# Kernel optimization log

Measured on AMD Instinct MI355X. Metric: run time of the kernel, lower is better.

## Reference

```python
import jax, jax.numpy as jnp
import numpy as np

BIG = 1e9
EPS_BETA = 1e-6
EPS_BN = 1e-5

N_NODES = 50000
N_EDGES = 800000
IN_DIM = 128
OUT_DIM = 128


def setup_inputs() -> dict:
    key = jax.random.key(0)
    ks = jax.random.split(key, 8)
    h = jax.random.normal(ks[0], (N_NODES, IN_DIM), dtype=jnp.float32)
    src = jax.random.randint(ks[1], (N_EDGES,), 0, N_NODES, dtype=jnp.int32)
    dst = jax.random.randint(ks[2], (N_EDGES,), 0, N_NODES, dtype=jnp.int32)
    sigma_GD = jax.random.uniform(ks[3], (N_EDGES,), dtype=jnp.float32)
    fc_w = jax.random.normal(ks[4], (IN_DIM, OUT_DIM), dtype=jnp.float32) / np.sqrt(IN_DIM)
    fc_b = jax.random.normal(ks[5], (OUT_DIM,), dtype=jnp.float32) * 0.01
    attn_w = jax.random.normal(ks[6], (2 * OUT_DIM, 1), dtype=jnp.float32) / np.sqrt(2 * OUT_DIM)
    attn_b = jax.random.normal(ks[7], (1,), dtype=jnp.float32) * 0.01
    bn_gamma = jnp.ones((OUT_DIM,), dtype=jnp.float32)
    bn_beta = jnp.zeros((OUT_DIM,), dtype=jnp.float32)
    return {"h": h, "src": src, "dst": dst, "sigma_GD": sigma_GD,
            "fc_w": fc_w, "fc_b": fc_b, "attn_w": attn_w, "attn_b": attn_b,
            "bn_gamma": bn_gamma, "bn_beta": bn_beta}


def reference(h, src, dst, sigma_GD, fc_w, fc_b, attn_w, attn_b, bn_gamma, bn_beta):
    n = h.shape[0]
    # node projection
    z = h @ fc_w + fc_b                                   # [N, D]
    z = jnp.where(jnp.isinf(z), BIG, z)
    # per-edge attention logits: concat(src,dst) @ W == src@W1 + dst@W2 (avoid concat materialization)
    d = z.shape[1]
    w_src, w_dst = attn_w[:d], attn_w[d:]
    z_src = z[src]                                        # [E, D]
    a = z_src @ w_src + z[dst] @ w_dst + attn_b           # [E, 1]
    a = jnp.where(jnp.isinf(a), BIG, a)
    e = jax.nn.leaky_relu(a, negative_slope=0.01)[:, 0]   # [E]
    # segment softmax over incoming edges (mailbox softmax)
    m = jax.ops.segment_max(e, dst, num_segments=n)       # [N]
    ex = jnp.exp(e - m[dst])
    denom = jax.ops.segment_sum(ex, dst, num_segments=n)  # [N]
    alpha = ex / denom[dst]                               # [E]
    # beta: sigma_GD normalized per destination node
    bsum = jax.ops.segment_sum(sigma_GD, dst, num_segments=n)
    beta = sigma_GD / (bsum[dst] + EPS_BETA)              # [E]
    # weighted scatter-sum of source features
    h_new = jax.ops.segment_sum((alpha * beta)[:, None] * z_src, dst, num_segments=n)  # [N, D]
    h_new = jnp.where(jnp.isinf(h_new), BIG, h_new)
    # BatchNorm1d (training-mode batch stats, biased variance, as torch does)
    mu = h_new.mean(axis=0)
    var = ((h_new - mu) ** 2).mean(axis=0)
    h_bn = (h_new - mu) * jax.lax.rsqrt(var + EPS_BN) * bn_gamma + bn_beta
    return jax.nn.elu(h_bn)
```

## Files before the change

kernel.cpp:

```cpp
#include <hip/hip_runtime.h>
#include <hip/hip_fp16.h>
#include <math.h>

#define N_NODES 50000
#define N_EDGES 800000
#define BIGV 1000000000.0f
#define NBLK_GEMM 3125
#define CHUNK 1024
#define NCHUNK 782
#define NCH4 784
#define NBUCKET 1563
#define NBK4 1564
#define BMAX 768
#define OVFSTRIDE 1024

typedef _Float16 half8 __attribute__((ext_vector_type(8)));
typedef float floatx4 __attribute__((ext_vector_type(4)));

__device__ __forceinline__ float clampinf(float x) { return isinf(x) ? BIGV : x; }

__device__ __forceinline__ void barrier_lgkm_only() {
    __builtin_amdgcn_sched_barrier(0);
    asm volatile("s_waitcnt lgkmcnt(0)" ::: "memory");
    __builtin_amdgcn_s_barrier();
    __builtin_amdgcn_sched_barrier(0);
}

__global__ __launch_bounds__(256) void k_prep(const float* __restrict__ W,
                                              __half* __restrict__ wt,
                                              float* __restrict__ bns,
                                              const int* __restrict__ dst,
                                              int* __restrict__ countsT)
{
    __shared__ int hist[NBK4];
    const int t = threadIdx.x;
    const int idx = blockIdx.x * 256 + t;
    if (idx < 16384) {
        int n = idx >> 7, k = idx & 127;
        wt[idx] = __float2half(W[k * 128 + n]);
    }
    if (idx < 256) bns[idx] = 0.f;
    for (int i = t; i < NBK4; i += 256) hist[i] = 0;
    __syncthreads();
    const int base = blockIdx.x * CHUNK;
    for (int i = t; i < CHUNK; i += 256) {
        int e = base + i;
        if (e < N_EDGES) atomicAdd(&hist[dst[e] >> 5], 1);
    }
    __syncthreads();
    for (int i = t; i < NBK4; i += 256)
        countsT[(size_t)i * NCH4 + blockIdx.x] = hist[i];
}

__global__ __launch_bounds__(256) void k_off(const int* __restrict__ countsT,
                                             int* __restrict__ cursC,
                                             int* __restrict__ btot)
{
    const int wv = (blockIdx.x << 2) + (threadIdx.x >> 6);
    const int l = threadIdx.x & 63;
    if (wv >= NBUCKET) {
        if (l == 0 && wv < NBK4) btot[wv] = 0;
        return;
    }
    const int* row = countsT + (size_t)wv * NCH4;
    int carry = 0;
    #pragma unroll
    for (int p = 0; p < 13; ++p) {
        const int c = p * 64 + l;
        const int v = (c < NCHUNK) ? row[c] : 0;
        int x = v;
        #pragma unroll
        for (int o = 1; o < 64; o <<= 1) {
            int u = __shfl_up(x, o);
            if (l >= o) x += u;
        }
        if (c < NCHUNK) cursC[(size_t)c * NBK4 + wv] = carry + x - v;
        carry += __shfl(x, 63);
    }
    if (l == 0) btot[wv] = carry;
}

__global__ __launch_bounds__(256) void k_gemm(
    const float* __restrict__ h, const __half* __restrict__ wt,
    const float* __restrict__ bias, const float* __restrict__ attn_w,
    __half* __restrict__ zh, float* __restrict__ sv, float* __restrict__ tv)
{
    __shared__ _Float16 hA[16][136];
    __shared__ float spart[4][16], tpart[4][16];

    const int tid = threadIdx.x;
    const int lane = tid & 63;
    const int wv = tid >> 6;
    const int l16 = lane & 15;
    const int oct = lane >> 4;
    const int n0 = wv << 5;
    const int node0 = blockIdx.x << 4;

    {
        const float4* h4 = (const float4*)(h + (size_t)node0 * 128);
        for (int i = tid; i < 512; i += 256) {
            int r = i >> 5, c4 = i & 31;
            float4 v = h4[i];
            union { __half2 h2[2]; uint2 u; } pk;
            pk.h2[0] = __floats2half2_rn(v.x, v.y);
            pk.h2[1] = __floats2half2_rn(v.z, v.w);
            *(uint2*)&hA[r][c4 << 2] = pk.u;
        }
    }

    half8 bfrag[4][2];
    #pragma unroll
    for (int kk = 0; kk < 4; ++kk)
        #pragma unroll
        for (int t = 0; t < 2; ++t)
            bfrag[kk][t] = *(const half8*)(wt + (size_t)(n0 + t * 16 + l16) * 128
                                              + kk * 32 + oct * 8);

    const float bv0 = bias[n0 + l16],         bv1 = bias[n0 + 16 + l16];
    const float ws0 = attn_w[n0 + l16],       ws1 = attn_w[n0 + 16 + l16];
    const float wd0 = attn_w[128 + n0 + l16], wd1 = attn_w[128 + n0 + 16 + l16];

    barrier_lgkm_only();

    floatx4 acc0 = {0.f, 0.f, 0.f, 0.f};
    floatx4 acc1 = {0.f, 0.f, 0.f, 0.f};
    #pragma unroll
    for (int kk = 0; kk < 4; ++kk) {
        half8 a = *(const half8*)&hA[l16][(kk << 5) + (oct << 3)];
        acc0 = __builtin_amdgcn_mfma_f32_16x16x32_f16(a, bfrag[kk][0], acc0, 0, 0, 0);
        acc1 = __builtin_amdgcn_mfma_f32_16x16x32_f16(a, bfrag[kk][1], acc1, 0, 0, 0);
    }

    float s_acc[4], t_acc[4];
    #pragma unroll
    for (int r = 0; r < 4; ++r) {
        float z0 = clampinf(acc0[r] + bv0);
        float z1 = clampinf(acc1[r] + bv1);
        const int row = (oct << 2) + r;
        zh[(size_t)(node0 + row) * 128 + n0 + l16]      = __float2half(z0);
        zh[(size_t)(node0 + row) * 128 + n0 + 16 + l16] = __float2half(z1);
        s_acc[r] = z0 * ws0 + z1 * ws1;
        t_acc[r] = z0 * wd0 + z1 * wd1;
    }
    #pragma unroll
    for (int r = 0; r < 4; ++r) {
        #pragma unroll
        for (int o = 1; o < 16; o <<= 1) {
            s_acc[r] += __shfl_xor(s_acc[r], o);
            t_acc[r] += __shfl_xor(t_acc[r], o);
        }
    }
    if (l16 == 0) {
        #pragma unroll
        for (int r = 0; r < 4; ++r) {
            spart[wv][(oct << 2) + r] = s_acc[r];
            tpart[wv][(oct << 2) + r] = t_acc[r];
        }
    }
    barrier_lgkm_only();
    if (tid < 16) {
        sv[node0 + tid] = spart[0][tid] + spart[1][tid] + spart[2][tid] + spart[3][tid];
        tv[node0 + tid] = tpart[0][tid] + tpart[1][tid] + tpart[2][tid] + tpart[3][tid];
    }
}

__global__ __launch_bounds__(512) void k_scat(
    const int* __restrict__ src, const int* __restrict__ dst,
    const float* __restrict__ sigma,
    const float* __restrict__ sv, const float* __restrict__ tv,
    const float* __restrict__ attn_b,
    const int* __restrict__ cursC, const int* __restrict__ btot,
    float4* __restrict__ tmp, int* __restrict__ bbase_g)
{
    __shared__ int cur[NBK4];
    __shared__ int bb[NBK4];
    __shared__ int tsc[512];
    const int t = threadIdx.x;
    const int self = blockIdx.x;

    for (int i = t; i < NBK4; i += 512) cur[i] = cursC[(size_t)self * NBK4 + i];

    uint4 bt = {0u, 0u, 0u, 0u};
    int tsum = 0;
    if (t < NBK4 / 4) {
        bt = ((const uint4*)btot)[t];
        tsum = (int)(bt.x + bt.y + bt.z + bt.w);
    }
    tsc[t] = tsum;
    __syncthreads();
    for (int off = 1; off < 512; off <<= 1) {
        int u = (t >= off) ? tsc[t - off] : 0;
        __syncthreads();
        tsc[t] += u;
        __syncthreads();
    }
    if (t < NBK4 / 4) {
        const int v0 = tsc[t] - tsum;
        bb[4*t+0] = v0;
        bb[4*t+1] = v0 + (int)bt.x;
        bb[4*t+2] = v0 + (int)bt.x + (int)bt.y;
        bb[4*t+3] = v0 + (int)bt.x + (int)bt.y + (int)bt.z;
    }
    __syncthreads();
    for (int i = t; i < NBK4; i += 512) cur[i] += bb[i];
    if (self == 0)
        for (int i = t; i < NBK4; i += 512) bbase_g[i] = bb[i];
    __syncthreads();

    const float ab = attn_b[0];
    const int base = self * CHUNK;
    for (int i = t; i < CHUNK; i += 512) {
        int e = base + i;
        if (e < N_EDGES) {
            int s = src[e];
            int d = dst[e];
            float a = sv[s] + tv[d] + ab;
            a = clampinf(a);
            float ev = a > 0.f ? a : 0.01f * a;
            int pos = atomicAdd(&cur[d >> 5], 1);
            float4 rec;
            rec.x = __int_as_float(s);
            rec.y = sigma[e];
            rec.z = ev;
            rec.w = __int_as_float(d);
            tmp[pos] = rec;
        }
    }
}

__global__ __launch_bounds__(512) void k_bagg(
    const float4* __restrict__ tmp, const int* __restrict__ bbase_g,
    const __half* __restrict__ zh, float4* __restrict__ ovf,
    float* __restrict__ out, float* __restrict__ partials)
{
    __shared__ float4 lrec[BMAX];
    __shared__ int hist[32];
    __shared__ int segs[33];
    __shared__ int cur[32];
    __shared__ float bnS[128], bnQ[128];
    const int t = threadIdx.x;
    const int b = blockIdx.x;
    const int s0 = bbase_g[b];
    const int n  = bbase_g[b + 1] - s0;

    if (t < 32) hist[t] = 0;
    if (t < 128) { bnS[t] = 0.f; bnQ[t] = 0.f; }
    __syncthreads();
    const float* tw = (const float*)tmp;
    for (int i = t; i < n; i += 512) {
        int d = __float_as_int(tw[4 * (size_t)(s0 + i) + 3]);
        atomicAdd(&hist[d & 31], 1);
    }
    __syncthreads();
    if (t < 32) {
        const int hv = hist[t];
        int x = hv;
        #pragma unroll
        for (int o = 1; o < 32; o <<= 1) {
            int u = __shfl_up(x, o);
            if (t >= o) x += u;
        }
        segs[t] = x - hv;
        cur[t]  = x - hv;
        if (t == 31) segs[32] = x;
    }
    __syncthreads();
    for (int i = t; i < n; i += 512) {
        float4 rec = tmp[s0 + i];
        int d = __float_as_int(rec.w);
        int pos = atomicAdd(&cur[d & 31], 1);
        if (pos < BMAX) lrec[pos] = rec;
        else            ovf[(size_t)b * OVFSTRIDE + (pos - BMAX)] = rec;
    }
    __syncthreads();

    const int lane = t & 63;
    const int wv = t >> 6;
    const int grp = lane >> 4;
    const int l16 = lane & 15;
    float pS[8] = {0.f,0.f,0.f,0.f,0.f,0.f,0.f,0.f};
    float pQ[8] = {0.f,0.f,0.f,0.f,0.f,0.f,0.f,0.f};

    for (int j = wv; j < 32; j += 8) {
        const int node = (b << 5) + j;
        if (node >= N_NODES) continue;
        const int beg = segs[j];
        const int deg = segs[j + 1] - beg;
        float acc[8] = {0.f,0.f,0.f,0.f,0.f,0.f,0.f,0.f};

        if (deg > 0) {
            if (deg <= 64) {
                int sidx = 0; float sig = 0.f, e = -INFINITY;
                if (lane < deg) {
                    const int off = beg + lane;
                    float4 r = (off < BMAX) ? lrec[off]
                             : ovf[(size_t)b * OVFSTRIDE + (off - BMAX)];
                    sidx = __float_as_int(r.x); sig = r.y; e = r.z;
                }
                float m = e;
                for (int o = 32; o; o >>= 1) m = fmaxf(m, __shfl_xor(m, o));
                float p = (lane < deg) ? __expf(e - m) : 0.f;
                float dn = p, bs = sig;
                for (int o = 32; o; o >>= 1) {
                    dn += __shfl_xor(dn, o);
                    bs += __shfl_xor(bs, o);
                }
                const float coef = p * sig * (1.0f / dn) / (bs + 1e-6f);
                for (int c = 0; c < deg; c += 8) {
                    const int j0 = c + grp, j1 = c + 4 + grp;
                    const int js0 = (j0 < deg) ? j0 : 0;
                    const int js1 = (j1 < deg) ? j1 : 0;
                    float cf0 = __shfl(coef, js0); int sj0 = __shfl(sidx, js0);
                    float cf1 = __shfl(coef, js1); int sj1 = __shfl(sidx, js1);
                    uint4 raw0, raw1;
                    if (j0 < deg)
                        raw0 = *(const uint4*)(zh + ((size_t)sj0 << 7) + (l16 << 3));
                    if (j1 < deg)
                        raw1 = *(const uint4*)(zh + ((size_t)sj1 << 7) + (l16 << 3));
                    if (j0 < deg) {
                        const __half2* hp = (const __half2*)&raw0;
                        #pragma unroll
                        for (int k = 0; k < 4; ++k) {
                            float2 f = __half22float2(hp[k]);
                            acc[2*k]   = fmaf(cf0, f.x, acc[2*k]);
                            acc[2*k+1] = fmaf(cf0, f.y, acc[2*k+1]);
                        }
                    }
                    if (j1 < deg) {
                        const __half2* hp = (const __half2*)&raw1;
                        #pragma unroll
                        for (int k = 0; k < 4; ++k) {
                            float2 f = __half22float2(hp[k]);
                            acc[2*k]   = fmaf(cf1, f.x, acc[2*k]);
                            acc[2*k+1] = fmaf(cf1, f.y, acc[2*k+1]);
                        }
                    }
                }
            } else {
                float m = -INFINITY;
                for (int i = lane; i < deg; i += 64) {
                    const int off = beg + i;
                    float4 r = (off < BMAX) ? lrec[off]
                             : ovf[(size_t)b * OVFSTRIDE + (off - BMAX)];
                    m = fmaxf(m, r.z);
                }
                for (int o = 32; o; o >>= 1) m = fmaxf(m, __shfl_xor(m, o));
                float dn = 0.f, bs = 0.f;
                for (int i = lane; i < deg; i += 64) {
                    const int off = beg + i;
                    float4 r = (off < BMAX) ? lrec[off]
                             : ovf[(size_t)b * OVFSTRIDE + (off - BMAX)];
                    dn += __expf(r.z - m); bs += r.y;
                }
                for (int o = 32; o; o >>= 1) {
                    dn += __shfl_xor(dn, o);
                    bs += __shfl_xor(bs, o);
                }
                const float scale = (1.0f / dn) / (bs + 1e-6f);
                for (int c = 0; c < deg; c += 64) {
                    int i = c + lane;
                    int sidx = 0; float coef = 0.f;
                    if (i < deg) {
                        const int off = beg + i;
                        float4 r = (off < BMAX) ? lrec[off]
                                 : ovf[(size_t)b * OVFSTRIDE + (off - BMAX)];
                        sidx = __float_as_int(r.x);
                        coef = __expf(r.z - m) * r.y * scale;
                    }
                    const int cnt2 = min(64, deg - c);
                    for (int jj = 0; jj < cnt2; jj += 4) {
                        const int j4 = jj + grp;
                        const int js = (j4 < cnt2) ? j4 : 0;
                        float cf = __shfl(coef, js);
                        int sj = __shfl(sidx, js);
                        if (j4 < cnt2) {
                            uint4 raw = *(const uint4*)(zh + ((size_t)sj << 7) + (l16 << 3));
                            const __half2* hp = (const __half2*)&raw;
                            #pragma unroll
                            for (int k = 0; k < 4; ++k) {
                                float2 f = __half22float2(hp[k]);
                                acc[2*k]   = fmaf(cf, f.x, acc[2*k]);
                                acc[2*k+1] = fmaf(cf, f.y, acc[2*k+1]);
                            }
                        }
                    }
                }
            }
        }
        #pragma unroll
        for (int k = 0; k < 8; ++k) {
            acc[k] += __shfl_xor(acc[k], 16);
            acc[k] += __shfl_xor(acc[k], 32);
        }
        if (grp == 0) {
            float o[8];
            #pragma unroll
            for (int k = 0; k < 8; ++k) {
                o[k] = clampinf(acc[k]);
                pS[k] += o[k];
                pQ[k] += o[k] * o[k];
            }
            float4 o0, o1;
            o0.x = o[0]; o0.y = o[1]; o0.z = o[2]; o0.w = o[3];
            o1.x = o[4]; o1.y = o[5]; o1.z = o[6]; o1.w = o[7];
            float4* op = (float4*)(out + (size_t)node * 128 + (l16 << 3));
            op[0] = o0; op[1] = o1;
        }
    }
    if (grp == 0) {
        #pragma unroll
        for (int k = 0; k < 8; ++k) {
            atomicAdd(&bnS[(l16 << 3) + k], pS[k]);
            atomicAdd(&bnQ[(l16 << 3) + k], pQ[k]);
        }
    }
    __syncthreads();
    if (t < 128) {
        partials[(size_t)b * 256 + t]       = bnS[t];
        partials[(size_t)b * 256 + 128 + t] = bnQ[t];
    }
}

__global__ __launch_bounds__(256) void k_bnred(const float* __restrict__ partials,
                                               float* __restrict__ bns)
{
    const int t = threadIdx.x;
    const int r0 = blockIdx.x * 25;
    const int r1 = min(r0 + 25, NBUCKET);
    float s = 0.f;
    for (int r = r0; r < r1; ++r) s += partials[(size_t)r * 256 + t];
    atomicAdd(&bns[t], s);
}

__global__ __launch_bounds__(256) void k_bnapply(float* __restrict__ io,
                                                 const float* __restrict__ sums,
                                                 const float* __restrict__ gamma,
                                                 const float* __restrict__ beta)
{
    __shared__ float sc[128], sh[128];
    const int tid = threadIdx.x;
    if (tid < 128) {
        const float invn = 1.0f / (float)N_NODES;
        float mu = sums[tid] * invn;
        float var = fmaxf(sums[128 + tid] * invn - mu * mu, 0.f);
        float g = gamma[tid] * rsqrtf(var + 1e-5f);
        sc[tid] = g;
        sh[tid] = beta[tid] - mu * g;
    }
    __syncthreads();
    const size_t idx = (size_t)blockIdx.x * 256 + tid;
    const int f4 = ((int)idx & 31) << 2;
    float4 x = ((const float4*)io)[idx];
    float y0 = x.x * sc[f4 + 0] + sh[f4 + 0];
    float y1 = x.y * sc[f4 + 1] + sh[f4 + 1];
    float y2 = x.z * sc[f4 + 2] + sh[f4 + 2];
    float y3 = x.w * sc[f4 + 3] + sh[f4 + 3];
    float4 o;
    o.x = y0 > 0.f ? y0 : expm1f(y0);
    o.y = y1 > 0.f ? y1 : expm1f(y1);
    o.z = y2 > 0.f ? y2 : expm1f(y2);
    o.w = y3 > 0.f ? y3 : expm1f(y3);
    ((float4*)io)[idx] = o;
}

extern "C" void kernel_launch(void* const* d_in, const int* in_sizes, int n_in,
                              void* d_out, int out_size, void* d_ws, size_t ws_size,
                              hipStream_t stream)
{
    const float* h      = (const float*)d_in[0];
    const int*   src    = (const int*)  d_in[1];
    const int*   dst    = (const int*)  d_in[2];
    const float* sigma  = (const float*)d_in[3];
    const float* fc_w   = (const float*)d_in[4];
    const float* fc_b   = (const float*)d_in[5];
    const float* attn_w = (const float*)d_in[6];
    const float* attn_b = (const float*)d_in[7];
    const float* gamma  = (const float*)d_in[8];
    const float* beta   = (const float*)d_in[9];
    float* out = (float*)d_out;

    float4* tmp    = (float4*)d_ws;
    float4* ovf    = tmp + N_EDGES;
    __half* zh     = (__half*)(ovf + (size_t)NBK4 * OVFSTRIDE);
    float*  sv     = (float*)(zh + (size_t)N_NODES * 128);
    float*  tv     = sv + N_NODES;
    float*  bns    = tv + N_NODES;
    float*  parts  = bns + 256;
    __half* wt     = (__half*)(parts + (size_t)NBK4 * 256);
    int*    countsT= (int*)(wt + 16384);
    int*    cursC  = countsT + (size_t)NBK4 * NCH4;
    int*    btot   = cursC + (size_t)NCH4 * NBK4;
    int*    bbase  = btot + NBK4;

    k_prep    <<<NCHUNK, 256, 0, stream>>>(fc_w, wt, bns, dst, countsT);
    k_off     <<<NBK4 / 4, 256, 0, stream>>>(countsT, cursC, btot);
    k_gemm    <<<NBLK_GEMM, 256, 0, stream>>>(h, wt, fc_b, attn_w, zh, sv, tv);
    k_scat    <<<NCHUNK, 512, 0, stream>>>(src, dst, sigma, sv, tv, attn_b,
                                           cursC, btot, tmp, bbase);
    k_bagg    <<<NBUCKET, 512, 0, stream>>>(tmp, bbase, zh, ovf, out, parts);
    k_bnred   <<<64, 256, 0, stream>>>(parts, bns);
    k_bnapply <<<(N_NODES * 128) / (256 * 4), 256, 0, stream>>>(out, bns, gamma, beta);
}
```

Measured before the change: 235.9 us.

## Move BN stats out of aggregation, unroll gather via LDS coefficients

Result: faster. 218.1 us (-7.5%).

```diff
diff --git a/kernel.cpp b/kernel.cpp
--- a/kernel.cpp
+++ b/kernel.cpp
@@ -13,6 +13,7 @@
 #define NBK4 1564
 #define BMAX 768
 #define OVFSTRIDE 1024
+#define NBLK_BN 512
 
 typedef _Float16 half8 __attribute__((ext_vector_type(8)));
 typedef float floatx4 __attribute__((ext_vector_type(4)));
@@ -231,20 +232,18 @@
 __global__ __launch_bounds__(512) void k_bagg(
     const float4* __restrict__ tmp, const int* __restrict__ bbase_g,
     const __half* __restrict__ zh, float4* __restrict__ ovf,
-    float* __restrict__ out, float* __restrict__ partials)
+    float* __restrict__ out)
 {
     __shared__ float4 lrec[BMAX];
     __shared__ int hist[32];
     __shared__ int segs[33];
     __shared__ int cur[32];
-    __shared__ float bnS[128], bnQ[128];
     const int t = threadIdx.x;
     const int b = blockIdx.x;
     const int s0 = bbase_g[b];
     const int n  = bbase_g[b + 1] - s0;
 
     if (t < 32) hist[t] = 0;
-    if (t < 128) { bnS[t] = 0.f; bnQ[t] = 0.f; }
     __syncthreads();
     const float* tw = (const float*)tmp;
     for (int i = t; i < n; i += 512) {
@@ -278,8 +277,6 @@
     const int wv = t >> 6;
     const int grp = lane >> 4;
     const int l16 = lane & 15;
-    float pS[8] = {0.f,0.f,0.f,0.f,0.f,0.f,0.f,0.f};
-    float pQ[8] = {0.f,0.f,0.f,0.f,0.f,0.f,0.f,0.f};
 
     for (int j = wv; j < 32; j += 8) {
         const int node = (b << 5) + j;
@@ -289,12 +286,10 @@
         float acc[8] = {0.f,0.f,0.f,0.f,0.f,0.f,0.f,0.f};
 
         if (deg > 0) {
-            if (deg <= 64) {
+            if (deg <= 64 && n <= BMAX) {
                 int sidx = 0; float sig = 0.f, e = -INFINITY;
                 if (lane < deg) {
-                    const int off = beg + lane;
-                    float4 r = (off < BMAX) ? lrec[off]
-                             : ovf[(size_t)b * OVFSTRIDE + (off - BMAX)];
+                    float4 r = lrec[beg + lane];
                     sidx = __float_as_int(r.x); sig = r.y; e = r.z;
                 }
                 float m = e;
@@ -306,33 +301,72 @@
                     bs += __shfl_xor(bs, o);
                 }
                 const float coef = p * sig * (1.0f / dn) / (bs + 1e-6f);
-                for (int c = 0; c < deg; c += 8) {
-                    const int j0 = c + grp, j1 = c + 4 + grp;
-                    const int js0 = (j0 < deg) ? j0 : 0;
-                    const int js1 = (j1 < deg) ? j1 : 0;
-                    float cf0 = __shfl(coef, js0); int sj0 = __shfl(sidx, js0);
-                    float cf1 = __shfl(coef, js1); int sj1 = __shfl(sidx, js1);
-                    uint4 raw0, raw1;
-                    if (j0 < deg)
-                        raw0 = *(const uint4*)(zh + ((size_t)sj0 << 7) + (l16 << 3));
-                    if (j1 < deg)
-                        raw1 = *(const uint4*)(zh + ((size_t)sj1 << 7) + (l16 << 3));
-                    if (j0 < deg) {
-                        const __half2* hp = (const __half2*)&raw0;
+                if (lane < deg) lrec[beg + lane].y = coef;
+                const int dm = deg - 1;
+                for (int c = 0; c < deg; c += 16) {
+                    const int j0 = c + grp, j1 = j0 + 4, j2 = j0 + 8, j3 = j0 + 12;
+                    float2 q0 = *(const float2*)&lrec[beg + min(j0, dm)];
+                    float2 q1 = *(const float2*)&lrec[beg + min(j1, dm)];
+                    float2 q2 = *(const float2*)&lrec[beg + min(j2, dm)];
+                    float2 q3 = *(const float2*)&lrec[beg + min(j3, dm)];
+                    uint4 r0 = *(const uint4*)(zh + ((size_t)__float_as_int(q0.x) << 7) + (l16 << 3));
+                    uint4 r1 = *(const uint4*)(zh + ((size_t)__float_as_int(q1.x) << 7) + (l16 << 3));
+                    uint4 r2 = *(const uint4*)(zh + ((size_t)__float_as_int(q2.x) << 7) + (l16 << 3));
+                    uint4 r3 = *(const uint4*)(zh + ((size_t)__float_as_int(q3.x) << 7) + (l16 << 3));
+                    const float c0 = (j0 < deg) ? q0.y : 0.f;
+                    const float c1 = (j1 < deg) ? q1.y : 0.f;
+                    const float c2 = (j2 < deg) ? q2.y : 0.f;
+                    const float c3 = (j3 < deg) ? q3.y : 0.f;
+                    const __half2* h0 = (const __half2*)&r0;
+                    const __half2* h1 = (const __half2*)&r1;
+                    const __half2* h2 = (const __half2*)&r2;
+                    const __half2* h3 = (const __half2*)&r3;
+                    #pragma unroll
+                    for (int k = 0; k < 4; ++k) {
+                        float2 f0 = __half22float2(h0[k]);
+                        float2 f1 = __half22float2(h1[k]);
+                        float2 f2 = __half22float2(h2[k]);
+                        float2 f3 = __half22float2(h3[k]);
+                        acc[2*k]   = fmaf(c0, f0.x, acc[2*k]);
+                        acc[2*k+1] = fmaf(c0, f0.y, acc[2*k+1]);
+                        acc[2*k]   = fmaf(c1, f1.x, acc[2*k]);
+                        acc[2*k+1] = fmaf(c1, f1.y, acc[2*k+1]);
+                        acc[2*k]   = fmaf(c2, f2.x, acc[2*k]);
+                        acc[2*k+1] = fmaf(c2, f2.y, acc[2*k+1]);
+                        acc[2*k]   = fmaf(c3, f3.x, acc[2*k]);
+                        acc[2*k+1] = fmaf(c3, f3.y, acc[2*k+1]);
+                    }
+                }
+            } else if (deg <= 64) {
+                int sidx = 0; float sig = 0.f, e = -INFINITY;
+                if (lane < deg) {
+                    const int off = beg + lane;
+                    float4 r = (off < BMAX) ? lrec[off]
+                             : ovf[(size_t)b * OVFSTRIDE + (off - BMAX)];
+                    sidx = __float_as_int(r.x); sig = r.y; e = r.z;
+                }
+                float m = e;
+                for (int o = 32; o; o >>= 1) m = fmaxf(m, __shfl_xor(m, o));
+                float p = (lane < deg) ? __expf(e - m) : 0.f;
+                float dn = p, bs = sig;
+                for (int o = 32; o; o >>= 1) {
+                    dn += __shfl_xor(dn, o);
+                    bs += __shfl_xor(bs, o);
+                }
+                const float coef = p * sig * (1.0f / dn) / (bs + 1e-6f);
+                for (int c = 0; c < deg; c += 4) {
+                    const int jj = c + grp;
+                    const int js = (jj < deg) ? jj : 0;
+                    float cf = __shfl(coef, js);
+                    int sj = __shfl(sidx, js);
+                    if (jj < deg) {
+                        uint4 raw = *(const uint4*)(zh + ((size_t)sj << 7) + (l16 << 3));
+                        const __half2* hp = (const __half2*)&raw;
                         #pragma unroll
                         for (int k = 0; k < 4; ++k) {
                             float2 f = __half22float2(hp[k]);
-                            acc[2*k]   = fmaf(cf0, f.x, acc[2*k]);
-                            acc[2*k+1] = fmaf(cf0, f.y, acc[2*k+1]);
-                        }
-                    }
-                    if (j1 < deg) {
-                        const __half2* hp = (const __half2*)&raw1;
-                        #pragma unroll
-                        for (int k = 0; k < 4; ++k) {
-                            float2 f = __half22float2(hp[k]);
-                            acc[2*k]   = fmaf(cf1, f.x, acc[2*k]);
-                            acc[2*k+1] = fmaf(cf1, f.y, acc[2*k+1]);
+                            acc[2*k]   = fmaf(cf, f.x, acc[2*k]);
+                            acc[2*k+1] = fmaf(cf, f.y, acc[2*k+1]);
                         }
                     }
                 }
@@ -393,43 +427,62 @@
             acc[k] += __shfl_xor(acc[k], 32);
         }
         if (grp == 0) {
-            float o[8];
-            #pragma unroll
-            for (int k = 0; k < 8; ++k) {
-                o[k] = clampinf(acc[k]);
-                pS[k] += o[k];
-                pQ[k] += o[k] * o[k];
-            }
             float4 o0, o1;
-            o0.x = o[0]; o0.y = o[1]; o0.z = o[2]; o0.w = o[3];
-            o1.x = o[4]; o1.y = o[5]; o1.z = o[6]; o1.w = o[7];
+            o0.x = clampinf(acc[0]); o0.y = clampinf(acc[1]);
+            o0.z = clampinf(acc[2]); o0.w = clampinf(acc[3]);
+            o1.x = clampinf(acc[4]); o1.y = clampinf(acc[5]);
+            o1.z = clampinf(acc[6]); o1.w = clampinf(acc[7]);
             float4* op = (float4*)(out + (size_t)node * 128 + (l16 << 3));
             op[0] = o0; op[1] = o1;
         }
     }
-    if (grp == 0) {
-        #pragma unroll
-        for (int k = 0; k < 8; ++k) {
-            atomicAdd(&bnS[(l16 << 3) + k], pS[k]);
-            atomicAdd(&bnQ[(l16 << 3) + k], pQ[k]);
-        }
-    }
-    __syncthreads();
-    if (t < 128) {
-        partials[(size_t)b * 256 + t]       = bnS[t];
-        partials[(size_t)b * 256 + 128 + t] = bnQ[t];
-    }
-}
-
-__global__ __launch_bounds__(256) void k_bnred(const float* __restrict__ partials,
-                                               float* __restrict__ bns)
-{
+}
+
+__global__ __launch_bounds__(256) void k_bnstats(const float* __restrict__ hnew,
+                                                 float* __restrict__ partials)
+{
+    const int tid = threadIdx.x;
+    const int f4 = (tid & 31) << 2;
+    const int rgrp = tid >> 5;
+    float4 s = {0.f, 0.f, 0.f, 0.f}, q = {0.f, 0.f, 0.f, 0.f};
+    for (int node = blockIdx.x * 8 + rgrp; node < N_NODES; node += NBLK_BN * 8) {
+        float4 v = *(const float4*)(hnew + (size_t)node * 128 + f4);
+        s.x += v.x; s.y += v.y; s.z += v.z; s.w += v.w;
+        q.x += v.x * v.x; q.y += v.y * v.y; q.z += v.z * v.z; q.w += v.w * v.w;
+    }
+    __shared__ float4 ls[256], lq[256];
+    ls[tid] = s; lq[tid] = q;
+    __syncthreads();
+    for (int off = 128; off >= 32; off >>= 1) {
+        if (tid < off) {
+            float4 a = ls[tid + off], b = lq[tid + off];
+            ls[tid].x += a.x; ls[tid].y += a.y; ls[tid].z += a.z; ls[tid].w += a.w;
+            lq[tid].x += b.x; lq[tid].y += b.y; lq[tid].z += b.z; lq[tid].w += b.w;
+        }
+        __syncthreads();
+    }
+    if (tid < 32) {
+        float* p = partials + (size_t)blockIdx.x * 256;
+        *(float4*)(p + f4)       = ls[tid];
+        *(float4*)(p + 128 + f4) = lq[tid];
+    }
+}
+
+__global__ __launch_bounds__(1024) void k_bnred(const float* __restrict__ partials,
+                                                float* __restrict__ sums)
+{
+    __shared__ float red[4][256];
     const int t = threadIdx.x;
-    const int r0 = blockIdx.x * 25;
-    const int r1 = min(r0 + 25, NBUCKET);
+    const int f = t & 255;
+    const int part = t >> 8;
     float s = 0.f;
-    for (int r = r0; r < r1; ++r) s += partials[(size_t)r * 256 + t];
-    atomicAdd(&bns[t], s);
+    #pragma unroll 8
+    for (int b = part * (NBLK_BN / 4); b < (part + 1) * (NBLK_BN / 4); ++b)
+        s += partials[(size_t)b * 256 + f];
+    red[part][f] = s;
+    __syncthreads();
+    if (part == 0)
+        sums[f] = red[0][f] + red[1][f] + red[2][f] + red[3][f];
 }
 
 __global__ __launch_bounds__(256) void k_bnapply(float* __restrict__ io,
@@ -486,7 +539,7 @@
     float*  tv     = sv + N_NODES;
     float*  bns    = tv + N_NODES;
     float*  parts  = bns + 256;
-    __half* wt     = (__half*)(parts + (size_t)NBK4 * 256);
+    __half* wt     = (__half*)(parts + (size_t)NBLK_BN * 256);
     int*    countsT= (int*)(wt + 16384);
     int*    cursC  = countsT + (size_t)NBK4 * NCH4;
     int*    btot   = cursC + (size_t)NCH4 * NBK4;
@@ -497,7 +550,8 @@
     k_gemm    <<<NBLK_GEMM, 256, 0, stream>>>(h, wt, fc_b, attn_w, zh, sv, tv);
     k_scat    <<<NCHUNK, 512, 0, stream>>>(src, dst, sigma, sv, tv, attn_b,
                                            cursC, btot, tmp, bbase);
-    k_bagg    <<<NBUCKET, 512, 0, stream>>>(tmp, bbase, zh, ovf, out, parts);
-    k_bnred   <<<64, 256, 0, stream>>>(parts, bns);
+    k_bagg    <<<NBUCKET, 512, 0, stream>>>(tmp, bbase, zh, ovf, out);
+    k_bnstats <<<NBLK_BN, 256, 0, stream>>>(out, parts);
+    k_bnred   <<<1, 1024, 0, stream>>>(parts, bns);
     k_bnapply <<<(N_NODES * 128) / (256 * 4), 256, 0, stream>>>(out, bns, gamma, beta);
 }
```
